# Performance work log

Measured on AMD Instinct MI355X. Metric: run time of the kernel, lower is better.

Reference implementation:

```python
import jax, jax.numpy as jnp
import numpy as np

BATCH, SEQ, IN, HID = 32, 1024, 512, 1024


def setup_inputs() -> dict:
    key = jax.random.key(0)
    std = 1.0 / np.sqrt(HID)
    ks = jax.random.split(key, 16)
    u = lambda k, shape: jax.random.uniform(k, shape, jnp.float32, -std, std)
    return {
        "x": jax.random.normal(ks[0], (BATCH, SEQ, IN), jnp.float32),
        "Wi": u(ks[1], (IN, 2 * HID)),
        "Wh": u(ks[2], (HID, 2 * HID)),
        "B": u(ks[3], (2 * HID,)),
        "Wni": u(ks[4], (IN, HID)),
        "Wnh": u(ks[5], (HID, HID)),
        "Bni": u(ks[6], (HID,)),
        "Bnh": u(ks[7], (HID,)),
        "Winvi": u(ks[8], (IN, 2 * HID)),
        "Winvh": u(ks[9], (HID, 2 * HID)),
        "Binv": u(ks[10], (2 * HID,)),
        "Wninvi": u(ks[11], (IN, HID)),
        "Wninvh": u(ks[12], (HID, HID)),
        "Bninvi": u(ks[13], (HID,)),
        "Bninvh": u(ks[14], (HID,)),
    }


def _gru_scan(x, Wi, Wh, Bg, Wni, Wnh, Bni, Bnh, reverse):
    # x: [B,S,I]; precompute input projections once (same math, batched GEMM)
    H = Wnh.shape[0]
    gi = jnp.einsum('bsi,ig->bsg', x, Wi) + Bg   # [B,S,2H]
    ni = jnp.einsum('bsi,ih->bsh', x, Wni) + Bni # [B,S,H]
    h0 = jnp.zeros((x.shape[0], H), x.dtype)

    def step(h, inp):
        g_t, n_t = inp                        # [B,2H], [B,H]
        gates = g_t + h @ Wh
        r = jax.nn.sigmoid(gates[:, :H])
        z = jax.nn.sigmoid(gates[:, H:])
        n = jnp.tanh(n_t + r * (h @ Wnh + Bnh))
        h = (1 - z) * n + z * h
        return h, h

    hT, hs = jax.lax.scan(step, h0, (gi.swapaxes(0, 1), ni.swapaxes(0, 1)),
                          reverse=reverse)
    return hs.swapaxes(0, 1), hT              # [B,S,H], [B,H]


def reference(x, Wi, Wh, B, Wni, Wnh, Bni, Bnh,
              Winvi, Winvh, Binv, Wninvi, Wninvh, Bninvi, Bninvh):
    out_f, h_f = _gru_scan(x, Wi, Wh, B, Wni, Wnh, Bni, Bnh, reverse=False)
    out_b, h_b = _gru_scan(x, Winvi, Winvh, Binv, Wninvi, Wninvh, Bninvi, Bninvh,
                           reverse=True)
    output = jnp.concatenate([out_f, out_b], axis=-1)  # [B,S,2H]
    ht = jnp.concatenate([h_f, h_b], axis=-1)          # [B,2H]
    return output, ht
```

## Files before the change

### kernel.cpp

```cpp
#include <hip/hip_runtime.h>
#include <cstdint>
#include <cstddef>

typedef __attribute__((ext_vector_type(8))) short s8v;
typedef __attribute__((ext_vector_type(4))) float f4v;
typedef __attribute__((ext_vector_type(4))) unsigned int u4v;

#define DEVFN __device__ __forceinline__

DEVFN unsigned short f2bf(float f) {
    unsigned int u = __builtin_bit_cast(unsigned int, f);
    return (unsigned short)((u + 0x7FFFu + ((u >> 16) & 1u)) >> 16);
}
DEVFN float bf2f(unsigned short h) {
    unsigned int u = ((unsigned int)h) << 16;
    return __builtin_bit_cast(float, u);
}
DEVFN float sigm(float x) { return 1.0f / (1.0f + __expf(-x)); }
DEVFN float tanh_fast(float x) { float e = __expf(2.0f * x); return 1.0f - 2.0f / (e + 1.0f); }

DEVFN void store_wt(unsigned int* p, unsigned int v) {
    asm volatile("global_store_dword %0, %1, off sc0 sc1"
                 :: "v"(p), "v"(v) : "memory");
}
DEVFN u4v poll_load4(const unsigned int* p) {
    u4v v;
    asm volatile("global_load_dwordx4 %0, %1, off sc0 sc1\n\t"
                 "s_waitcnt vmcnt(0)"
                 : "=v"(v) : "v"(p) : "memory");
    return v;
}
DEVFN void gather_h(const void* p0, const void* p1,
                    u4v& a0, u4v& a1, u4v& a2, u4v& a3,
                    u4v& a4, u4v& a5, u4v& a6, u4v& a7) {
    asm volatile(
        "global_load_dwordx4 %0, %8, off sc0 sc1\n\t"
        "global_load_dwordx4 %1, %8, off offset:1024 sc0 sc1\n\t"
        "global_load_dwordx4 %2, %8, off offset:2048 sc0 sc1\n\t"
        "global_load_dwordx4 %3, %8, off offset:3072 sc0 sc1\n\t"
        "global_load_dwordx4 %4, %9, off sc0 sc1\n\t"
        "global_load_dwordx4 %5, %9, off offset:1024 sc0 sc1\n\t"
        "global_load_dwordx4 %6, %9, off offset:2048 sc0 sc1\n\t"
        "global_load_dwordx4 %7, %9, off offset:3072 sc0 sc1\n\t"
        "s_waitcnt vmcnt(0)"
        : "=&v"(a0), "=&v"(a1), "=&v"(a2), "=&v"(a3),
          "=&v"(a4), "=&v"(a5), "=&v"(a6), "=&v"(a7)
        : "v"(p0), "v"(p1)
        : "memory");
}

constexpr int BB = 32, SS = 1024, II = 512, HH = 1024;
constexpr int NCOL = 6144;

constexpr size_t OFF_X    = 0;
constexpr size_t SZ_X     = (size_t)BB * SS * II * 2;
constexpr size_t OFF_WINT = OFF_X + SZ_X;
constexpr size_t SZ_WINT  = (size_t)NCOL * II * 2;
constexpr size_t OFF_WREC = OFF_WINT + SZ_WINT;
constexpr size_t SZ_WREC  = (size_t)2 * 3072 * HH * 2;
constexpr size_t OFF_BIAS = OFF_WREC + SZ_WREC;
constexpr size_t SZ_BIAS  = (size_t)NCOL * 4;
constexpr size_t OFF_H    = OFF_BIAS + SZ_BIAS;
constexpr size_t SZ_H     = (size_t)2 * 2 * 2 * 64 * 512;
constexpr size_t OFF_BAR  = OFF_H + SZ_H;
constexpr size_t SZ_BAR   = 4096;
constexpr size_t OFF_G    = OFF_BAR + SZ_BAR;
constexpr size_t SZ_G     = (size_t)SS * BB * NCOL * 2;
constexpr size_t WS_NEED  = OFF_G + SZ_G;

constexpr int WL_OFF = 0;
constexpr int PL_OFF = 98304;
constexpr int GR_OFF = 124416;
constexpr int PF_OFF = 130560;
constexpr int RD_OFF = 130592;
constexpr int PG_OFF = 130608;
constexpr int OB_OFF = 130624;
constexpr int SMEM_TOT = 147008;
constexpr int PLF = 4 * 3 * 16 * 17;

__global__ void prep_kernel(
    const float* __restrict__ x,
    const float* __restrict__ Wi, const float* __restrict__ Wni,
    const float* __restrict__ Winvi, const float* __restrict__ Wninvi,
    const float* __restrict__ Wh, const float* __restrict__ Wnh,
    const float* __restrict__ Winvh, const float* __restrict__ Wninvh,
    const float* __restrict__ Bg, const float* __restrict__ Bni,
    const float* __restrict__ Binv, const float* __restrict__ Bninvi,
    unsigned short* __restrict__ xb, unsigned short* __restrict__ WinT,
    unsigned short* __restrict__ Wrec, float* __restrict__ bias)
{
    typedef __attribute__((ext_vector_type(4))) unsigned int uv4;
    constexpr int NX8 = (BB * SS * II) / 8;
    constexpr int NWI = NCOL * II;
    constexpr int NWR = NCOL * HH;
    constexpr int TOT = NX8 + NWI + NWR + NCOL;
    for (int i = blockIdx.x * blockDim.x + threadIdx.x; i < TOT;
         i += gridDim.x * blockDim.x) {
        if (i < NX8) {
            const float* sp = x + (size_t)i * 8;
            unsigned short o[8];
#pragma unroll
            for (int j = 0; j < 8; ++j) o[j] = f2bf(sp[j]);
            uv4 v;
            v[0] = (unsigned)o[0] | ((unsigned)o[1] << 16);
            v[1] = (unsigned)o[2] | ((unsigned)o[3] << 16);
            v[2] = (unsigned)o[4] | ((unsigned)o[5] << 16);
            v[3] = (unsigned)o[6] | ((unsigned)o[7] << 16);
            *(uv4*)(xb + (size_t)i * 8) = v;
        } else if (i < NX8 + NWI) {
            int u = i - NX8;
            int k = u / NCOL, n = u % NCOL;
            const float* src; int stride, col;
            if (n < 2048)      { src = Wi;     col = n;        stride = 2048; }
            else if (n < 3072) { src = Wni;    col = n - 2048; stride = 1024; }
            else if (n < 5120) { src = Winvi;  col = n - 3072; stride = 2048; }
            else               { src = Wninvi; col = n - 5120; stride = 1024; }
            WinT[(size_t)n * 512 + k] = f2bf(src[(size_t)k * stride + col]);
        } else if (i < NX8 + NWI + NWR) {
            int u = i - NX8 - NWI;
            int k = u / NCOL, R = u % NCOL;
            int dir = R / 3072, rr = R % 3072;
            const float* src; int stride, col;
            if (rr < 2048) { src = dir ? Winvh : Wh;   col = rr;        stride = 2048; }
            else           { src = dir ? Wninvh : Wnh; col = rr - 2048; stride = 1024; }
            Wrec[(size_t)R * 1024 + k] = f2bf(src[(size_t)k * stride + col]);
        } else {
            int c = i - NX8 - NWI - NWR;
            int dir = c / 3072, cc = c % 3072;
            bias[c] = (cc < 2048) ? (dir ? Binv : Bg)[cc]
                                  : (dir ? Bninvi : Bni)[cc - 2048];
        }
    }
}

#define GLL16(gp, lp) __builtin_amdgcn_global_load_lds( \
    (const __attribute__((address_space(1))) void*)(gp), \
    (__attribute__((address_space(3))) void*)(lp), 16, 0, 0)

__global__ __launch_bounds__(256, 2) void gemm_in(
    const unsigned short* __restrict__ xb,
    const unsigned short* __restrict__ WinT,
    const float* __restrict__ bias,
    unsigned short* __restrict__ G)
{
    __shared__ char smem[65536];
    const int tid = threadIdx.x, lane = tid & 63, wid = tid >> 6;
    int wg = blockIdx.x;
    int swz = (wg & 7) * 1536 + (wg >> 3);
    const int m0 = (swz & 255) * 128, n0 = (swz >> 8) * 128;
    const int l15 = lane & 15, hi = lane >> 4;
    const int mw = (wid & 1) * 64, nw = (wid >> 1) * 64;

    f4v acc[4][4] = {};
    const char* xrow = (const char*)xb;
    const char* wrow = (const char*)WinT;

    auto stage = [&](int buf, int kt) {
        char* As = smem + buf * 32768;
        char* Bs = As + 16384;
        const int kb0 = kt * 128;
#pragma unroll
        for (int r = 0; r < 4; ++r) {
            int q = wid * 4 + r;
            int o = q * 1024 + lane * 16;
            int row = o >> 7;
            int kbs = (o ^ ((row & 7) << 4)) & 127;
            GLL16(xrow + (size_t)(m0 + row) * 1024 + kb0 + kbs, As + q * 1024);
            GLL16(wrow + (size_t)(n0 + row) * 1024 + kb0 + kbs, Bs + q * 1024);
        }
    };

    stage(0, 0);
    __syncthreads();
    int buf = 0;
    for (int kt = 0; kt < 8; ++kt) {
        if (kt < 7) stage(buf ^ 1, kt + 1);
        char* As = smem + buf * 32768;
        char* Bs = As + 16384;
#pragma unroll
        for (int kc = 0; kc < 2; ++kc) {
            s8v a[4], b[4];
#pragma unroll
            for (int mt = 0; mt < 4; ++mt) {
                int row = mw + mt * 16 + l15;
                int off = (row << 7) + kc * 64 + hi * 16;
                a[mt] = *(const s8v*)(As + (off ^ ((row & 7) << 4)));
            }
#pragma unroll
            for (int nt = 0; nt < 4; ++nt) {
                int row = nw + nt * 16 + l15;
                int off = (row << 7) + kc * 64 + hi * 16;
                b[nt] = *(const s8v*)(Bs + (off ^ ((row & 7) << 4)));
            }
#pragma unroll
            for (int mt = 0; mt < 4; ++mt)
#pragma unroll
                for (int nt = 0; nt < 4; ++nt)
                    acc[mt][nt] = __builtin_amdgcn_mfma_f32_16x16x32_bf16(
                        a[mt], b[nt], acc[mt][nt], 0, 0, 0);
        }
        __syncthreads();
        buf ^= 1;
    }
#pragma unroll
    for (int mt = 0; mt < 4; ++mt) {
#pragma unroll
        for (int rg = 0; rg < 4; ++rg) {
            int m = m0 + mw + mt * 16 + hi * 4 + rg;
            int bi = m >> 10, si = m & 1023;
            int bg = bi >> 4, b16 = bi & 15;
#pragma unroll
            for (int nt = 0; nt < 4; ++nt) {
                int n = n0 + nw + nt * 16 + l15;
                int dir = (n >= 3072);
                int rem = n - dir * 3072;
                int gate = rem >> 10, col = rem & 1023;
                int jg = col >> 4, j = col & 15;
                size_t idx = (((((size_t)si * 2 + dir) * 64 + jg) * 2 + bg) * 16
                              + b16) * 48 + gate * 16 + j;
                G[idx] = f2bf(acc[mt][nt][rg] + bias[n]);
            }
        }
    }
}

__global__ __launch_bounds__(320, 1) void gru_rec(
    const unsigned short* __restrict__ G,
    const unsigned short* __restrict__ Wrec,
    const float* __restrict__ Bnh,
    const float* __restrict__ Bninvh,
    unsigned short* __restrict__ hbuf,
    float* __restrict__ out,
    unsigned int* __restrict__ flags)
{
    extern __shared__ char smem[];
    char* wl = smem + WL_OFF;
    float* pl = (float*)(smem + PL_OFF);
    unsigned short* gring = (unsigned short*)(smem + GR_OFF);
    volatile int* pflag = (volatile int*)(smem + PF_OFF);
    volatile int* gready = (volatile int*)(smem + RD_OFF);
    volatile int* gprog  = (volatile int*)(smem + PG_OFF);
    float* obuf = (float*)(smem + OB_OFF);

    const int tid = threadIdx.x, lane = tid & 63, wid = tid >> 6;
    const int bid = blockIdx.x;
    const int dir = bid >> 7, bg = (bid >> 6) & 1, jg = bid & 63;
    const int jbase = jg * 16, bb = bg * 16;
    const int l15 = lane & 15, hi = lane >> 4;
    unsigned int* fl = flags + ((dir * 2 + bg) << 8);

    if (tid < 4) { gready[tid] = -1; gprog[tid] = -1; }
    if (tid >= 4 && tid < 12) pflag[tid - 4] = -1;
    if (tid < 256) {
        const char* wsrc = (const char*)Wrec;
        for (int q = 0; q < 24; ++q) {
            int o = (q * 256 + tid) * 16;
            int c = o >> 11;
            int kb = (o ^ ((c & 7) << 4)) & 2047;
            int n = dir * 3072 + (c >> 4) * 1024 + jbase + (c & 15);
            *(u4v*)(wl + o) = *(const u4v*)(wsrc + (size_t)n * 2048 + kb);
        }
    }
    const int b_l = tid >> 4, j_l = tid & 15;
    const float bnh = (dir ? Bninvh : Bnh)[jbase + (j_l & 15)];
    __syncthreads();

    const size_t gstride_b = (size_t)2 * 64 * 2 * 768 * 2;
    const char* gcb = (const char*)G + (((size_t)dir * 64 + jg) * 2 + bg) * 1536;

    if (wid == 4) {
        char* grb = (char*)gring;
        for (int t = 0; t < 1024; ++t) {
            const int slot = t & 3;
            if (t >= 4) {
                int v;
                do { v = gprog[lane & 3]; } while (!__all(v >= t - 4));
            }
            const int gpos = dir ? (1023 - t) : t;
            const char* src = gcb + (size_t)gpos * gstride_b + lane * 32;
            if (lane < 48) {
                u4v d0 = *(const u4v*)(src);
                u4v d1 = *(const u4v*)(src + 16);
                *(u4v*)(grb + slot * 1536 + lane * 32) = d0;
                *(u4v*)(grb + slot * 1536 + lane * 32 + 16) = d1;
            }
            asm volatile("s_waitcnt lgkmcnt(0) vmcnt(0)" ::: "memory");
            if (lane == 0) gready[slot] = t;
        }
        return;
    }

    float h_old = 0.0f;
    unsigned int* hbuf32 = (unsigned int*)hbuf;

    for (int s = 0; s < 1024; ++s) {
        const int par = s & 1;
        float* plc = pl + par * PLF;

        const int slot = s & 3;
        {
            int r;
            do { r = gready[slot]; } while (r != s);
        }
        asm volatile("" ::: "memory");
        const int gb = slot * 768 + b_l * 48 + j_l;
        unsigned short gr = gring[gb];
        unsigned short gz = gring[gb + 16];
        unsigned short gn = gring[gb + 32];
        asm volatile("s_waitcnt lgkmcnt(0)" ::: "memory");
        if (lane == 0) gprog[wid] = s;

        float rsum = 0.f, zsum = 0.f, nsum = 0.f;
        if (s > 0) {
            const unsigned tgt = (unsigned)s;
            const unsigned int* fp = fl + (lane << 2);
            u4v fv;
            do {
                fv = poll_load4(fp);
            } while (!__all(fv[0] >= tgt && fv[1] >= tgt &&
                            fv[2] >= tgt && fv[3] >= tgt));

            const int rbuf = par ^ 1;
            const char* hb = (const char*)hbuf +
                ((((size_t)(dir * 2 + rbuf) * 2 + bg) * 64)
                 + (size_t)(wid * 16 + (hi >> 1))) * 512
                + l15 * 32 + (hi & 1) * 16;
            u4v u[8];
            gather_h(hb, hb + 4096, u[0], u[1], u[2], u[3],
                     u[4], u[5], u[6], u[7]);

            f4v acc[3] = {};
#pragma unroll
            for (int p = 0; p < 3; ++p) {
                int c = p * 16 + l15;
                int cbase = c << 11;
                int sw = (c & 7) << 4;
#pragma unroll
                for (int kc = 0; kc < 8; ++kc) {
                    int off = cbase + (wid << 9) + kc * 64 + hi * 16;
                    s8v bf = *(const s8v*)(wl + (off ^ sw));
                    acc[p] = __builtin_amdgcn_mfma_f32_16x16x32_bf16(
                        __builtin_bit_cast(s8v, u[kc]), bf, acc[p], 0, 0, 0);
                }
            }
#pragma unroll
            for (int p = 0; p < 3; ++p)
#pragma unroll
                for (int rg = 0; rg < 4; ++rg)
                    plc[((wid * 3 + p) * 16 + hi * 4 + rg) * 17 + l15] = acc[p][rg];
            asm volatile("s_waitcnt lgkmcnt(0)" ::: "memory");
            if (lane == 0) pflag[par * 4 + wid] = s;

            {
                int f0, f1, f2, f3;
                do {
                    f0 = pflag[par * 4 + 0]; f1 = pflag[par * 4 + 1];
                    f2 = pflag[par * 4 + 2]; f3 = pflag[par * 4 + 3];
                } while (f0 < s || f1 < s || f2 < s || f3 < s);
            }
            asm volatile("" ::: "memory");
#pragma unroll
            for (int w = 0; w < 4; ++w) {
                rsum += plc[((w * 3 + 0) * 16 + b_l) * 17 + j_l];
                zsum += plc[((w * 3 + 1) * 16 + b_l) * 17 + j_l];
                nsum += plc[((w * 3 + 2) * 16 + b_l) * 17 + j_l];
            }
        }

        float rv = sigm(rsum + bf2f(gr));
        float zv = sigm(zsum + bf2f(gz));
        float nv = tanh_fast(bf2f(gn) + rv * (nsum + bnh));
        float hn = (1.0f - zv) * nv + zv * h_old;
        h_old = hn;

        if (s < 1023) {
            unsigned short hbv = f2bf(hn);
            unsigned int other = (unsigned int)(unsigned short)__shfl_xor((int)hbv, 1);
            if (!(tid & 1)) {
                size_t w32 = ((((size_t)(dir * 2 + par) * 2 + bg) * 64 + jg) * 128)
                             + b_l * 8 + (j_l >> 1);
                store_wt(hbuf32 + w32, (unsigned)hbv | (other << 16));
            }
            asm volatile("s_waitcnt vmcnt(0)" ::: "memory");
            if (lane == 0)
                store_wt(&fl[jg * 4 + wid], (unsigned)(s + 1));
        }

        obuf[(s & 15) * 256 + tid] = hn;
        if ((s & 15) == 15) {
            const int s0 = s - 15;
#pragma unroll
            for (int k = 0; k < 16; ++k) {
                float v = obuf[k * 256 + tid];
                int st = s0 + k;
                int s_out = dir ? (1023 - st) : st;
                __builtin_nontemporal_store(v,
                    &out[((size_t)(bb + b_l) * SS + s_out) * 2048
                         + dir * 1024 + jbase + j_l]);
            }
        }
        if (s == 1023)
            __builtin_nontemporal_store(hn,
                &out[(size_t)BB * SS * 2048 + (size_t)(bb + b_l) * 2048 +
                     dir * 1024 + jbase + j_l]);
    }
}

extern "C" void kernel_launch(void* const* d_in, const int* in_sizes, int n_in,
                              void* d_out, int out_size, void* d_ws, size_t ws_size,
                              hipStream_t stream)
{
    if (n_in < 15) return;
    const float* x      = (const float*)d_in[0];
    const float* Wi     = (const float*)d_in[1];
    const float* Wh     = (const float*)d_in[2];
    const float* Bg     = (const float*)d_in[3];
    const float* Wni    = (const float*)d_in[4];
    const float* Wnh    = (const float*)d_in[5];
    const float* Bni    = (const float*)d_in[6];
    const float* Bnh    = (const float*)d_in[7];
    const float* Winvi  = (const float*)d_in[8];
    const float* Winvh  = (const float*)d_in[9];
    const float* Binv   = (const float*)d_in[10];
    const float* Wninvi = (const float*)d_in[11];
    const float* Wninvh = (const float*)d_in[12];
    const float* Bninvi = (const float*)d_in[13];
    const float* Bninvh = (const float*)d_in[14];

    if (ws_size < WS_NEED) {
        hipMemsetAsync(d_out, 0, (size_t)out_size * 4, stream);
        return;
    }
    char* ws = (char*)d_ws;
    unsigned short* xb   = (unsigned short*)(ws + OFF_X);
    unsigned short* WinT = (unsigned short*)(ws + OFF_WINT);
    unsigned short* Wrec = (unsigned short*)(ws + OFF_WREC);
    float*          bias = (float*)(ws + OFF_BIAS);
    unsigned short* hbuf = (unsigned short*)(ws + OFF_H);
    unsigned int*   bar  = (unsigned int*)(ws + OFF_BAR);
    unsigned short* G    = (unsigned short*)(ws + OFF_G);

    hipMemsetAsync(ws + OFF_BAR, 0, SZ_BAR, stream);

    prep_kernel<<<4096, 256, 0, stream>>>(
        x, Wi, Wni, Winvi, Wninvi, Wh, Wnh, Winvh, Wninvh,
        Bg, Bni, Binv, Bninvi, xb, WinT, Wrec, bias);

    gemm_in<<<12288, 256, 0, stream>>>(xb, WinT, bias, G);

    hipFuncSetAttribute(reinterpret_cast<const void*>(&gru_rec),
                        hipFuncAttributeMaxDynamicSharedMemorySize, SMEM_TOT);
    gru_rec<<<256, 320, SMEM_TOT, stream>>>(
        G, Wrec, Bnh, Bninvh, hbuf, (float*)d_out, bar);
}
```

Measured before the change: 4.301 ms.

## Issue flag poll early, skip self wait, and coalesce gate-projection stores via LDS

The recurrent kernel now issues its flag load right after publishing its own flag, so the first check at the next step can often skip a fresh round trip. Each lane watches one producer flag, and lanes whose producer is their own group are excluded from the wait. Separately, the input-projection GEMM epilogue stages its bf16 results in shared memory and writes them to the gate buffer as 16-byte vector stores instead of scattered 2-byte stores. The per-lane mapping of flags and the new store index arithmetic must exactly match the layout the recurrence expects, which is easy to get wrong.

```diff
diff --git a/kernel.cpp b/kernel.cpp
--- a/kernel.cpp
+++ b/kernel.cpp
@@ -23,12 +23,16 @@
     asm volatile("global_store_dword %0, %1, off sc0 sc1"
                  :: "v"(p), "v"(v) : "memory");
 }
-DEVFN u4v poll_load4(const unsigned int* p) {
-    u4v v;
-    asm volatile("global_load_dwordx4 %0, %1, off sc0 sc1\n\t"
+DEVFN unsigned poll_load(const unsigned int* p) {
+    unsigned v;
+    asm volatile("global_load_dword %0, %1, off sc0 sc1\n\t"
                  "s_waitcnt vmcnt(0)"
                  : "=v"(v) : "v"(p) : "memory");
     return v;
+}
+DEVFN void poll_issue(const unsigned int* p, unsigned& v) {
+    asm volatile("global_load_dword %0, %1, off sc0 sc1"
+                 : "=v"(v) : "v"(p) : "memory");
 }
 DEVFN void gather_h(const void* p0, const void* p1,
                     u4v& a0, u4v& a1, u4v& a2, u4v& a3,
@@ -202,24 +206,40 @@
         __syncthreads();
         buf ^= 1;
     }
-#pragma unroll
-    for (int mt = 0; mt < 4; ++mt) {
-#pragma unroll
-        for (int rg = 0; rg < 4; ++rg) {
-            int m = m0 + mw + mt * 16 + hi * 4 + rg;
-            int bi = m >> 10, si = m & 1023;
-            int bg = bi >> 4, b16 = bi & 15;
-#pragma unroll
-            for (int nt = 0; nt < 4; ++nt) {
-                int n = n0 + nw + nt * 16 + l15;
-                int dir = (n >= 3072);
-                int rem = n - dir * 3072;
-                int gate = rem >> 10, col = rem & 1023;
-                int jg = col >> 4, j = col & 15;
-                size_t idx = (((((size_t)si * 2 + dir) * 64 + jg) * 2 + bg) * 16
-                              + b16) * 48 + gate * 16 + j;
-                G[idx] = f2bf(acc[mt][nt][rg] + bias[n]);
-            }
+
+    {
+        unsigned short* cs = (unsigned short*)smem;
+#pragma unroll
+        for (int mt = 0; mt < 4; ++mt)
+#pragma unroll
+            for (int rg = 0; rg < 4; ++rg) {
+                int sil = mw + mt * 16 + hi * 4 + rg;
+#pragma unroll
+                for (int nt = 0; nt < 4; ++nt) {
+                    int n = n0 + nw + nt * 16 + l15;
+                    int jgl = (nw >> 4) + nt;
+                    cs[(sil * 8 + jgl) * 16 + l15] =
+                        f2bf(acc[mt][nt][rg] + bias[n]);
+                }
+            }
+        __syncthreads();
+        const int n_dir = (n0 >= 3072);
+        const int rem0 = n0 - n_dir * 3072;
+        const int gate = rem0 >> 10;
+        const int jg0 = (rem0 & 1023) >> 4;
+        const int bi = m0 >> 10;
+        const int bgb = bi >> 4, b16 = bi & 15;
+        const int si0 = m0 & 1023;
+        const char* lbase = (const char*)cs;
+#pragma unroll
+        for (int r = 0; r < 8; ++r) {
+            int uidx = r * 256 + tid;
+            int piece = uidx >> 1, half = uidx & 1;
+            int sil = piece >> 3, jgl = piece & 7;
+            u4v d = *(const u4v*)(lbase + piece * 32 + half * 16);
+            size_t gb = (((((size_t)(si0 + sil) * 2 + n_dir) * 64 + (jg0 + jgl))
+                          * 2 + bgb) * 16 + b16) * 96 + gate * 32 + half * 16;
+            *(u4v*)((char*)G + gb) = d;
         }
     }
 }
@@ -292,6 +312,9 @@
 
     float h_old = 0.0f;
     unsigned int* hbuf32 = (unsigned int*)hbuf;
+    const unsigned int* fp = fl + wid * 64 + lane;
+    const bool self = (wid * 16 + (lane >> 2)) == jg;
+    unsigned early_v = 0;
 
     for (int s = 0; s < 1024; ++s) {
         const int par = s & 1;
@@ -313,12 +336,11 @@
         float rsum = 0.f, zsum = 0.f, nsum = 0.f;
         if (s > 0) {
             const unsigned tgt = (unsigned)s;
-            const unsigned int* fp = fl + (lane << 2);
-            u4v fv;
-            do {
-                fv = poll_load4(fp);
-            } while (!__all(fv[0] >= tgt && fv[1] >= tgt &&
-                            fv[2] >= tgt && fv[3] >= tgt));
+            asm volatile("s_waitcnt vmcnt(0) ; %0" : "+v"(early_v) :: "memory");
+            if (!__all(self | (early_v >= tgt))) {
+                unsigned v;
+                do { v = poll_load(fp); } while (!__all(self | (v >= tgt)));
+            }
 
             const int rbuf = par ^ 1;
             const char* hb = (const char*)hbuf +
@@ -384,6 +406,7 @@
             asm volatile("s_waitcnt vmcnt(0)" ::: "memory");
             if (lane == 0)
                 store_wt(&fl[jg * 4 + wid], (unsigned)(s + 1));
+            poll_issue(fp, early_v);
         }
 
         obuf[(s & 15) * 256 + tid] = hn;
```

New measurement: 5.685 ms. 32.2% more time.
